# Optimization experiments

Hardware: AMD Instinct MI355X
Metric: run time of the kernel (lower is better)

Reference implementation:

```python
import jax, jax.numpy as jnp
import numpy as np

D_MODEL = 768
N_HEADS = 12
D_HEAD = D_MODEL // N_HEADS

def setup_inputs() -> dict:
    key = jax.random.key(0)
    ks = jax.random.split(key, 5)
    B, T = 2, 4096
    x = jax.random.normal(ks[0], (B, T, D_MODEL), dtype=jnp.float32)
    s_in = 1.0 / np.sqrt(D_MODEL)
    W_qkv = jax.random.normal(ks[1], (D_MODEL, 3 * D_MODEL), dtype=jnp.float32) * s_in
    b_qkv = jnp.zeros((3 * D_MODEL,), dtype=jnp.float32)
    W_proj = jax.random.normal(ks[2], (D_MODEL, D_MODEL), dtype=jnp.float32) * s_in
    b_proj = jnp.zeros((D_MODEL,), dtype=jnp.float32)
    return {"x": x, "W_qkv": W_qkv, "b_qkv": b_qkv, "W_proj": W_proj, "b_proj": b_proj}

def reference(x, W_qkv, b_qkv, W_proj, b_proj):
    B, T, C = x.shape
    qkv = x @ W_qkv + b_qkv                      # [B,T,3C]
    q, k, v = jnp.split(qkv, 3, axis=-1)
    def heads(t):
        return t.reshape(B, T, N_HEADS, D_HEAD).transpose(0, 2, 1, 3)  # [B,H,T,d]
    q, k, v = heads(q), heads(k), heads(v)
    scale = 1.0 / np.sqrt(D_HEAD)
    att = jnp.einsum('bhqd,bhkd->bhqk', q, k) * scale  # [B,H,T,T]
    causal = jnp.tril(jnp.ones((T, T), dtype=bool))
    att = jnp.where(causal[None, None], att, -jnp.inf)
    att = jax.nn.softmax(att, axis=-1)
    y = jnp.einsum('bhqk,bhkd->bhqd', att, v)          # [B,H,T,d]
    y = y.transpose(0, 2, 1, 3).reshape(B, T, C)
    return y @ W_proj + b_proj
```

## Files before the change

kernel.cpp:

```cpp
#include <hip/hip_runtime.h>
#include <hip/hip_bf16.h>

typedef __bf16 bf16_t;
typedef bf16_t bf16x4 __attribute__((ext_vector_type(4)));
typedef bf16_t bf16x8 __attribute__((ext_vector_type(8)));
typedef float  f32x4  __attribute__((ext_vector_type(4)));

#define TSEQ   4096
#define NBATCH 2
#define DMODEL 768
#define NHEADS 12
#define DHEAD  64
#define NTOK   (NBATCH*TSEQ)
#define NQKV   (3*DMODEL)

#define QSCALE 0.18033688011112042f
#define SMAX 24.0f

__device__ __forceinline__ f32x4 mfma16(bf16x8 a, bf16x8 b, f32x4 c) {
  return __builtin_amdgcn_mfma_f32_16x16x32_bf16(a, b, c, 0, 0, 0);
}

__device__ __forceinline__ void glds16(const bf16_t* g, bf16_t* l) {
  __builtin_amdgcn_global_load_lds(
      (const __attribute__((address_space(1))) void*)g,
      (__attribute__((address_space(3))) void*)l, 16, 0, 0);
}

__global__ __launch_bounds__(256) void k_prep(
    const float* __restrict__ W1, bf16_t* __restrict__ O1,
    const float* __restrict__ W2, bf16_t* __restrict__ O2,
    const float* __restrict__ X, bf16_t* __restrict__ Xb) {
  __shared__ bf16_t tile[64][66];
  int t = blockIdx.x;
  if (t >= 576) {
    const int idx = (t - 576) * 256 + threadIdx.x;
#pragma unroll
    for (int it = 0; it < 2; ++it) {
      const long c = (long)idx + (long)it * 393216;
      const float4 v0 = *(const float4*)(X + c * 8);
      const float4 v1 = *(const float4*)(X + c * 8 + 4);
      bf16x8 o;
      o[0] = (bf16_t)v0.x; o[1] = (bf16_t)v0.y;
      o[2] = (bf16_t)v0.z; o[3] = (bf16_t)v0.w;
      o[4] = (bf16_t)v1.x; o[5] = (bf16_t)v1.y;
      o[6] = (bf16_t)v1.z; o[7] = (bf16_t)v1.w;
      *(bf16x8*)(Xb + c * 8) = o;
    }
    return;
  }
  const float* in; bf16_t* out; int R, C, c0, r0;
  if (t < 432) { in = W1; out = O1; R = DMODEL; C = NQKV;
                 c0 = (t % 36) * 64; r0 = (t / 36) * 64; }
  else { t -= 432; in = W2; out = O2; R = DMODEL; C = DMODEL;
         c0 = (t % 12) * 64; r0 = (t / 12) * 64; }
  const int tid = threadIdx.x;
  const int r = tid >> 2, cb = (tid & 3) * 16;
  const float* ip = in + (long)(r0 + r) * C + c0 + cb;
#pragma unroll
  for (int k = 0; k < 16; k += 4) {
    float4 v = *(const float4*)(ip + k);
    tile[r][cb + k + 0] = (bf16_t)v.x;
    tile[r][cb + k + 1] = (bf16_t)v.y;
    tile[r][cb + k + 2] = (bf16_t)v.z;
    tile[r][cb + k + 3] = (bf16_t)v.w;
  }
  __syncthreads();
  const int c = tid >> 2, rb = (tid & 3) * 16;
  bf16_t* op = out + (long)(c0 + c) * R + r0 + rb;
  bf16x8 v0, v1;
#pragma unroll
  for (int i = 0; i < 8; ++i) { v0[i] = tile[rb + i][c]; v1[i] = tile[rb + 8 + i][c]; }
  *(bf16x8*)(op) = v0;
  *(bf16x8*)(op + 8) = v1;
}

__global__ __launch_bounds__(256) void k_gemm_qkv(
    const bf16_t* __restrict__ Xb, const bf16_t* __restrict__ Bt,
    const float* __restrict__ bias,
    bf16_t* __restrict__ Qo, bf16_t* __restrict__ Ko, bf16_t* __restrict__ Vt) {
  __shared__ __align__(16) bf16_t As[2 * 128 * 32];
  __shared__ __align__(16) bf16_t Bs[2 * 128 * 32];
  const int wave = threadIdx.x >> 6;
  const int lane = threadIdx.x & 63;
  const int quad = lane >> 4;
  const int l16  = lane & 15;
  const int m0 = blockIdx.x * 128;
  const int n0 = blockIdx.y * 128;

  const int srow4  = lane >> 2;
  const int schunk = (lane & 3) ^ ((lane >> 3) & 3);
  const bf16_t* a0 = Xb + (long)(m0 + wave * 32 + srow4) * DMODEL + schunk * 8;
  const bf16_t* b0 = Bt + (long)(n0 + wave * 32 + srow4) * DMODEL + schunk * 8;

  f32x4 acc[2][8] = {};

  glds16(a0,               As + (wave * 32) * 32);
  glds16(a0 + 16 * DMODEL, As + (wave * 32 + 16) * 32);
  glds16(b0,               Bs + (wave * 32) * 32);
  glds16(b0 + 16 * DMODEL, Bs + (wave * 32 + 16) * 32);
  __syncthreads();

  const int sw = (l16 >> 1) & 3;
  for (int ks = 0; ks < DMODEL / 32; ++ks) {
    const int p = ks & 1;
    if (ks + 1 < DMODEL / 32) {
      const int k1 = (ks + 1) * 32;
      bf16_t* Asx = (p ? As : As + 128 * 32);
      bf16_t* Bsx = (p ? Bs : Bs + 128 * 32);
      glds16(a0 + k1,               Asx + (wave * 32) * 32);
      glds16(a0 + 16 * DMODEL + k1, Asx + (wave * 32 + 16) * 32);
      glds16(b0 + k1,               Bsx + (wave * 32) * 32);
      glds16(b0 + 16 * DMODEL + k1, Bsx + (wave * 32 + 16) * 32);
    }
    const bf16_t* Ap = As + p * (128 * 32);
    const bf16_t* Bp = Bs + p * (128 * 32);

    bf16x8 af0 = *(const bf16x8*)(Ap + (wave * 32 + l16) * 32 + ((quad ^ sw) << 3));
    bf16x8 af1 = *(const bf16x8*)(Ap + (wave * 32 + 16 + l16) * 32 + ((quad ^ sw) << 3));
#pragma unroll
    for (int nt = 0; nt < 8; ++nt) {
      bf16x8 bfm = *(const bf16x8*)(Bp + (nt * 16 + l16) * 32 + ((quad ^ sw) << 3));
      acc[0][nt] = mfma16(af0, bfm, acc[0][nt]);
      acc[1][nt] = mfma16(af1, bfm, acc[1][nt]);
    }
    __syncthreads();
  }

#pragma unroll
  for (int s = 0; s < 2; ++s)
#pragma unroll
    for (int nt = 0; nt < 8; ++nt) {
      const int n = n0 + nt * 16 + l16;
      const float bv = bias[n];
      const int mb = m0 + wave * 32 + s * 16 + quad * 4;
      const int b = mb >> 12;
      const int t = mb & 4095;
      if (n < DMODEL) {
        const int h = n >> 6, d = n & 63;
        bf16_t* qp = Qo + (((long)(b * NHEADS + h) * TSEQ + t) << 6) + d;
#pragma unroll
        for (int j = 0; j < 4; ++j)
          qp[(long)j << 6] = (bf16_t)((acc[s][nt][j] + bv) * QSCALE);
      } else if (n < 2 * DMODEL) {
        const int n2 = n - DMODEL, h = n2 >> 6, d = n2 & 63;
        bf16_t* kp = Ko + (((long)(b * NHEADS + h) * TSEQ + t) << 6) + d;
#pragma unroll
        for (int j = 0; j < 4; ++j)
          kp[(long)j << 6] = (bf16_t)(acc[s][nt][j] + bv);
      } else {
        const int n2 = n - 2 * DMODEL, h = n2 >> 6, d = n2 & 63;
        bf16x4 v;
#pragma unroll
        for (int j = 0; j < 4; ++j) v[j] = (bf16_t)(acc[s][nt][j] + bv);
        *(bf16x4*)(Vt + ((long)(b * NHEADS + h) * DHEAD + d) * TSEQ + t) = v;
      }
    }
}

__global__ __launch_bounds__(256) void k_combine(
    const bf16_t* __restrict__ P0, const bf16_t* __restrict__ P1,
    const float* __restrict__ L0, const float* __restrict__ L1,
    bf16_t* __restrict__ Ab) {
  const int bh = blockIdx.x;
  const int t  = blockIdx.y * 32 + (threadIdx.x >> 3);
  const int d0 = (threadIdx.x & 7) * 8;
  const long lidx = (long)bh * TSEQ + t;
  const float li = 1.f / (L0[lidx] + L1[lidx]);
  const long pidx = (lidx << 6) + d0;
  bf16x8 a = *(const bf16x8*)(P0 + pidx);
  bf16x8 b = *(const bf16x8*)(P1 + pidx);
  bf16x8 o;
#pragma unroll
  for (int j = 0; j < 8; ++j)
    o[j] = (bf16_t)(((float)a[j] + (float)b[j]) * li);
  const int bb = bh / NHEADS, h = bh % NHEADS;
  *(bf16x8*)(Ab + (long)(bb * TSEQ + t) * DMODEL + h * 64 + d0) = o;
}

__global__ __launch_bounds__(256) void k_gemm_proj(
    const bf16_t* __restrict__ Ab, const bf16_t* __restrict__ Bt,
    const float* __restrict__ bias, float* __restrict__ out) {
  __shared__ __align__(16) bf16_t As[2 * 128 * 32];
  __shared__ __align__(16) bf16_t Bs[2 * 128 * 32];
  const int wave = threadIdx.x >> 6;
  const int lane = threadIdx.x & 63;
  const int quad = lane >> 4;
  const int l16  = lane & 15;
  const int m0 = blockIdx.x * 128;
  const int n0 = blockIdx.y * 128;

  const int srow4  = lane >> 2;
  const int schunk = (lane & 3) ^ ((lane >> 3) & 3);
  const bf16_t* a0 = Ab + (long)(m0 + wave * 32 + srow4) * DMODEL + schunk * 8;
  const bf16_t* b0 = Bt + (long)(n0 + wave * 32 + srow4) * DMODEL + schunk * 8;

  f32x4 acc[2][8] = {};

  glds16(a0,               As + (wave * 32) * 32);
  glds16(a0 + 16 * DMODEL, As + (wave * 32 + 16) * 32);
  glds16(b0,               Bs + (wave * 32) * 32);
  glds16(b0 + 16 * DMODEL, Bs + (wave * 32 + 16) * 32);
  __syncthreads();

  const int sw = (l16 >> 1) & 3;
  for (int ks = 0; ks < DMODEL / 32; ++ks) {
    const int p = ks & 1;
    if (ks + 1 < DMODEL / 32) {
      const int k1 = (ks + 1) * 32;
      bf16_t* Asx = (p ? As : As + 128 * 32);
      bf16_t* Bsx = (p ? Bs : Bs + 128 * 32);
      glds16(a0 + k1,               Asx + (wave * 32) * 32);
      glds16(a0 + 16 * DMODEL + k1, Asx + (wave * 32 + 16) * 32);
      glds16(b0 + k1,               Bsx + (wave * 32) * 32);
      glds16(b0 + 16 * DMODEL + k1, Bsx + (wave * 32 + 16) * 32);
    }
    const bf16_t* Ap = As + p * (128 * 32);
    const bf16_t* Bp = Bs + p * (128 * 32);

    bf16x8 af0 = *(const bf16x8*)(Ap + (wave * 32 + l16) * 32 + ((quad ^ sw) << 3));
    bf16x8 af1 = *(const bf16x8*)(Ap + (wave * 32 + 16 + l16) * 32 + ((quad ^ sw) << 3));
#pragma unroll
    for (int nt = 0; nt < 8; ++nt) {
      bf16x8 bfm = *(const bf16x8*)(Bp + (nt * 16 + l16) * 32 + ((quad ^ sw) << 3));
      acc[0][nt] = mfma16(af0, bfm, acc[0][nt]);
      acc[1][nt] = mfma16(af1, bfm, acc[1][nt]);
    }
    __syncthreads();
  }

#pragma unroll
  for (int s = 0; s < 2; ++s)
#pragma unroll
    for (int nt = 0; nt < 8; ++nt) {
      const int n = n0 + nt * 16 + l16;
      const float bv = bias[n];
      const int m = m0 + wave * 32 + s * 16 + quad * 4;
#pragma unroll
      for (int j = 0; j < 4; ++j)
        out[(long)(m + j) * DMODEL + n] = acc[s][nt][j] + bv;
    }
}

__global__ __launch_bounds__(256, 4) void k_attn(
    const bf16_t* __restrict__ Q, const bf16_t* __restrict__ K,
    const bf16_t* __restrict__ Vt,
    bf16_t* __restrict__ P0, bf16_t* __restrict__ P1,
    float* __restrict__ L0, float* __restrict__ L1) {
  __shared__ __align__(16) bf16_t kbuf[2][64 * 64];
  __shared__ __align__(16) bf16_t vbuf[2][64 * 64];
  const int wave = threadIdx.x >> 6;
  const int lane = threadIdx.x & 63;
  const int quad = lane >> 4;
  const int l16  = lane & 15;
  const int bh = blockIdx.x;
  const int qt = 31 - (blockIdx.y >> 1);
  const int sp = blockIdx.y & 1;
  const int niter = qt + 1;
  const int c0 = sp * niter;
  bf16_t* Pp = sp ? P1 : P0;
  float*  Lp = sp ? L1 : L0;

  const bf16_t* Qh = Q + ((long)bh * TSEQ << 6);
  const bf16_t* Kh = K + ((long)bh * TSEQ << 6);
  const bf16_t* Vh = Vt + (long)bh * DHEAD * TSEQ;

  const int qbase = qt * 128 + wave * 32;

  bf16x8 qf[2][2];
#pragma unroll
  for (int s = 0; s < 2; ++s) {
    const bf16_t* qrow = Qh + ((long)(qbase + s * 16 + l16) << 6);
    qf[s][0] = *(const bf16x8*)(qrow + quad * 8);
    qf[s][1] = *(const bf16x8*)(qrow + 32 + quad * 8);
  }

  f32x4 acc[2][4] = {};
  float lS[2] = {0.f, 0.f};
  const f32x4 minit = {-SMAX, -SMAX, -SMAX, -SMAX};

  const int kperm = ((l16 >> 2) << 3) + (l16 & 3);
  const int swl = l16 & 7;
  const int srow = lane >> 3;
  const int cV = (lane & 7) ^ (srow & 7);
  const int cK0 = (lane & 7) ^ (srow & 3);
  const int cK1 = cK0 ^ 4;
  const int r0a = wave * 16, r0b = wave * 16 + 8;

  {
    const int k00 = c0 << 6;
    glds16(Kh + ((long)(k00 + r0a + srow) << 6) + cK0 * 8, &kbuf[0][r0a * 64]);
    glds16(Kh + ((long)(k00 + r0b + srow) << 6) + cK1 * 8, &kbuf[0][r0b * 64]);
    glds16(Vh + (long)(r0a + srow) * TSEQ + k00 + cV * 8,  &vbuf[0][r0a * 64]);
    glds16(Vh + (long)(r0b + srow) * TSEQ + k00 + cV * 8,  &vbuf[0][r0b * 64]);
  }
  __syncthreads();

  for (int ci = 0; ci < niter; ++ci) {
    const int p = ci & 1;
    const int k0 = (c0 + ci) << 6;
    if (ci + 1 < niter) {
      const int k1 = k0 + 64;
      glds16(Kh + ((long)(k1 + r0a + srow) << 6) + cK0 * 8, &kbuf[1 - p][r0a * 64]);
      glds16(Kh + ((long)(k1 + r0b + srow) << 6) + cK1 * 8, &kbuf[1 - p][r0b * 64]);
      glds16(Vh + (long)(r0a + srow) * TSEQ + k1 + cV * 8,  &vbuf[1 - p][r0a * 64]);
      glds16(Vh + (long)(r0b + srow) * TSEQ + k1 + cV * 8,  &vbuf[1 - p][r0b * 64]);
    }
    const bf16_t* kb = kbuf[p];
    const bf16_t* vb = vbuf[p];

#pragma unroll
    for (int g = 0; g < 2; ++g) {
      const int rw0 = (g * 32 + kperm) * 64;
      const int rw1 = (g * 32 + 4 + kperm) * 64;
      bf16x8 kf00 = *(const bf16x8*)(kb + rw0 + ((quad ^ swl) << 3));
      bf16x8 kf01 = *(const bf16x8*)(kb + rw0 + (((quad + 4) ^ swl) << 3));
      bf16x8 kf10 = *(const bf16x8*)(kb + rw1 + ((quad ^ swl) << 3));
      bf16x8 kf11 = *(const bf16x8*)(kb + rw1 + (((quad + 4) ^ swl) << 3));
      const bool domask = (k0 + g * 32 + 31 > qbase);

      bf16x8 pf[2];
#pragma unroll
      for (int s = 0; s < 2; ++s) {
        f32x4 st0 = minit, st1 = minit;
        st0 = mfma16(kf00, qf[s][0], st0);
        st0 = mfma16(kf01, qf[s][1], st0);
        st1 = mfma16(kf10, qf[s][0], st1);
        st1 = mfma16(kf11, qf[s][1], st1);
        if (domask) {
          const int qS = qbase + s * 16 + l16;
          const int kb0 = k0 + g * 32 + quad * 8;
#pragma unroll
          for (int j = 0; j < 4; ++j) {
            if (kb0 + j > qS)     st0[j] = -1e30f;
            if (kb0 + 4 + j > qS) st1[j] = -1e30f;
          }
        }
        float rs = 0.f;
#pragma unroll
        for (int j = 0; j < 4; ++j) {
          float e0 = __builtin_amdgcn_exp2f(st0[j]);
          float e1 = __builtin_amdgcn_exp2f(st1[j]);
          rs += e0 + e1;
          pf[s][j]     = (bf16_t)e0;
          pf[s][4 + j] = (bf16_t)e1;
        }
        lS[s] += rs;
      }
#pragma unroll
      for (int dt = 0; dt < 4; ++dt) {
        const int row = dt * 16 + l16;
        bf16x8 vf = *(const bf16x8*)(vb + row * 64 + ((((g << 2) + quad) ^ swl) << 3));
#pragma unroll
        for (int s = 0; s < 2; ++s)
          acc[s][dt] = mfma16(vf, pf[s], acc[s][dt]);
      }
    }
    __syncthreads();
  }

#pragma unroll
  for (int s = 0; s < 2; ++s) {
    lS[s] += __shfl_xor(lS[s], 16);
    lS[s] += __shfl_xor(lS[s], 32);
  }
#pragma unroll
  for (int s = 0; s < 2; ++s) {
    const int qS = qbase + s * 16 + l16;
    bf16_t* prow = Pp + (((long)bh * TSEQ + qS) << 6);
#pragma unroll
    for (int dt = 0; dt < 4; ++dt) {
      bf16x4 w;
#pragma unroll
      for (int j = 0; j < 4; ++j) w[j] = (bf16_t)acc[s][dt][j];
      *(bf16x4*)(prow + dt * 16 + quad * 4) = w;
    }
    if (quad == 0) Lp[(long)bh * TSEQ + qS] = lS[s];
  }
}

extern "C" void kernel_launch(void* const* d_in, const int* in_sizes, int n_in,
                              void* d_out, int out_size, void* d_ws, size_t ws_size,
                              hipStream_t stream) {
  (void)in_sizes; (void)n_in; (void)out_size; (void)ws_size;
  const float* x     = (const float*)d_in[0];
  const float* Wqkv  = (const float*)d_in[1];
  const float* bqkv  = (const float*)d_in[2];
  const float* Wproj = (const float*)d_in[3];
  const float* bproj = (const float*)d_in[4];
  float* out = (float*)d_out;

  char* ws = (char*)d_ws;
  bf16_t* wqkv_t  = (bf16_t*)ws; ws += (long)NQKV * DMODEL * 2;
  bf16_t* wproj_t = (bf16_t*)ws; ws += (long)DMODEL * DMODEL * 2;
  bf16_t* Xb      = (bf16_t*)ws; ws += (long)NTOK * DMODEL * 2;
  bf16_t* Qb      = (bf16_t*)ws; ws += (long)NTOK * DMODEL * 2;
  bf16_t* Kb      = (bf16_t*)ws; ws += (long)NTOK * DMODEL * 2;
  bf16_t* Vtb     = (bf16_t*)ws; ws += (long)NTOK * DMODEL * 2;
  bf16_t* P0b     = (bf16_t*)ws; ws += (long)NTOK * DMODEL * 2;
  bf16_t* P1b     = (bf16_t*)ws; ws += (long)NTOK * DMODEL * 2;
  bf16_t* Abb     = (bf16_t*)ws; ws += (long)NTOK * DMODEL * 2;
  float*  L0b     = (float*)ws;  ws += (long)NHEADS * NBATCH * TSEQ * 4;
  float*  L1b     = (float*)ws;  ws += (long)NHEADS * NBATCH * TSEQ * 4;

  k_prep<<<576 + 1536, 256, 0, stream>>>(Wqkv, wqkv_t, Wproj, wproj_t, x, Xb);
  k_gemm_qkv<<<dim3(NTOK / 128, NQKV / 128), 256, 0, stream>>>(Xb, wqkv_t, bqkv, Qb, Kb, Vtb);
  k_attn<<<dim3(NBATCH * NHEADS, 64), 256, 0, stream>>>(Qb, Kb, Vtb, P0b, P1b, L0b, L1b);
  k_combine<<<dim3(NBATCH * NHEADS, TSEQ / 32), 256, 0, stream>>>(
      P0b, P1b, L0b, L1b, Abb);
  k_gemm_proj<<<dim3(NTOK / 128, DMODEL / 128), 256, 0, stream>>>(
      Abb, wproj_t, bproj, out);
}
```

Measured before the change: 221.9 us.

## Drop split-KV attention with combine kernel; triple-buffer QKV GEMM loads

The attention kernel no longer splits each query tile's causal KV range across two blocks. Each block now processes the whole range and normalizes its output directly into the projection input, which removes the combine kernel and the partial-output and log-sum buffers. Separately, the QKV GEMM moves from double to triple-buffered LDS staging with explicit vmcnt waits and raw barriers, so loads for the next two k-slices stay in flight. The cost is half as many attention blocks (768 versus 1536) with long, unbalanced per-block work, so tail imbalance and lower occupancy may hurt.

```diff
diff --git a/kernel.cpp b/kernel.cpp
--- a/kernel.cpp
+++ b/kernel.cpp
@@ -79,6 +79,99 @@
     const bf16_t* __restrict__ Xb, const bf16_t* __restrict__ Bt,
     const float* __restrict__ bias,
     bf16_t* __restrict__ Qo, bf16_t* __restrict__ Ko, bf16_t* __restrict__ Vt) {
+  __shared__ __align__(16) bf16_t As[3 * 128 * 32];
+  __shared__ __align__(16) bf16_t Bs[3 * 128 * 32];
+  const int wave = threadIdx.x >> 6;
+  const int lane = threadIdx.x & 63;
+  const int quad = lane >> 4;
+  const int l16  = lane & 15;
+  const int m0 = blockIdx.x * 128;
+  const int n0 = blockIdx.y * 128;
+
+  const int srow4  = lane >> 2;
+  const int schunk = (lane & 3) ^ ((lane >> 3) & 3);
+  const bf16_t* a0 = Xb + (long)(m0 + wave * 32 + srow4) * DMODEL + schunk * 8;
+  const bf16_t* b0 = Bt + (long)(n0 + wave * 32 + srow4) * DMODEL + schunk * 8;
+
+  f32x4 acc[2][8] = {};
+
+  auto stage = [&](int ks) {
+    const int koff = ks * 32;
+    bf16_t* Ax = As + (ks % 3) * (128 * 32);
+    bf16_t* Bx = Bs + (ks % 3) * (128 * 32);
+    glds16(a0 + koff,               Ax + (wave * 32) * 32);
+    glds16(a0 + 16 * DMODEL + koff, Ax + (wave * 32 + 16) * 32);
+    glds16(b0 + koff,               Bx + (wave * 32) * 32);
+    glds16(b0 + 16 * DMODEL + koff, Bx + (wave * 32 + 16) * 32);
+  };
+
+  const int NS = DMODEL / 32;
+  stage(0);
+  stage(1);
+  asm volatile("s_waitcnt vmcnt(4)" ::: "memory");
+  __builtin_amdgcn_s_barrier();
+  __builtin_amdgcn_sched_barrier(0);
+
+  const int sw = (l16 >> 1) & 3;
+  for (int ks = 0; ks < NS; ++ks) {
+    if (ks + 2 < NS) stage(ks + 2);
+    const bf16_t* Ap = As + (ks % 3) * (128 * 32);
+    const bf16_t* Bp = Bs + (ks % 3) * (128 * 32);
+
+    bf16x8 af0 = *(const bf16x8*)(Ap + (wave * 32 + l16) * 32 + ((quad ^ sw) << 3));
+    bf16x8 af1 = *(const bf16x8*)(Ap + (wave * 32 + 16 + l16) * 32 + ((quad ^ sw) << 3));
+#pragma unroll
+    for (int nt = 0; nt < 8; ++nt) {
+      bf16x8 bfm = *(const bf16x8*)(Bp + (nt * 16 + l16) * 32 + ((quad ^ sw) << 3));
+      acc[0][nt] = mfma16(af0, bfm, acc[0][nt]);
+      acc[1][nt] = mfma16(af1, bfm, acc[1][nt]);
+    }
+
+    if (ks + 1 < NS) {
+      if (ks + 2 < NS) {
+        asm volatile("s_waitcnt vmcnt(4)" ::: "memory");
+      } else {
+        asm volatile("s_waitcnt vmcnt(0)" ::: "memory");
+      }
+      __builtin_amdgcn_s_barrier();
+      __builtin_amdgcn_sched_barrier(0);
+    }
+  }
+
+#pragma unroll
+  for (int s = 0; s < 2; ++s)
+#pragma unroll
+    for (int nt = 0; nt < 8; ++nt) {
+      const int n = n0 + nt * 16 + l16;
+      const float bv = bias[n];
+      const int mb = m0 + wave * 32 + s * 16 + quad * 4;
+      const int b = mb >> 12;
+      const int t = mb & 4095;
+      if (n < DMODEL) {
+        const int h = n >> 6, d = n & 63;
+        bf16_t* qp = Qo + (((long)(b * NHEADS + h) * TSEQ + t) << 6) + d;
+#pragma unroll
+        for (int j = 0; j < 4; ++j)
+          qp[(long)j << 6] = (bf16_t)((acc[s][nt][j] + bv) * QSCALE);
+      } else if (n < 2 * DMODEL) {
+        const int n2 = n - DMODEL, h = n2 >> 6, d = n2 & 63;
+        bf16_t* kp = Ko + (((long)(b * NHEADS + h) * TSEQ + t) << 6) + d;
+#pragma unroll
+        for (int j = 0; j < 4; ++j)
+          kp[(long)j << 6] = (bf16_t)(acc[s][nt][j] + bv);
+      } else {
+        const int n2 = n - 2 * DMODEL, h = n2 >> 6, d = n2 & 63;
+        bf16x4 v;
+#pragma unroll
+        for (int j = 0; j < 4; ++j) v[j] = (bf16_t)(acc[s][nt][j] + bv);
+        *(bf16x4*)(Vt + ((long)(b * NHEADS + h) * DHEAD + d) * TSEQ + t) = v;
+      }
+    }
+}
+
+__global__ __launch_bounds__(256) void k_gemm_proj(
+    const bf16_t* __restrict__ Ab, const bf16_t* __restrict__ Bt,
+    const float* __restrict__ bias, float* __restrict__ out) {
   __shared__ __align__(16) bf16_t As[2 * 128 * 32];
   __shared__ __align__(16) bf16_t Bs[2 * 128 * 32];
   const int wave = threadIdx.x >> 6;
@@ -90,7 +183,7 @@
 
   const int srow4  = lane >> 2;
   const int schunk = (lane & 3) ^ ((lane >> 3) & 3);
-  const bf16_t* a0 = Xb + (long)(m0 + wave * 32 + srow4) * DMODEL + schunk * 8;
+  const bf16_t* a0 = Ab + (long)(m0 + wave * 32 + srow4) * DMODEL + schunk * 8;
   const bf16_t* b0 = Bt + (long)(n0 + wave * 32 + srow4) * DMODEL + schunk * 8;
 
   f32x4 acc[2][8] = {};
@@ -133,108 +226,6 @@
     for (int nt = 0; nt < 8; ++nt) {
       const int n = n0 + nt * 16 + l16;
       const float bv = bias[n];
-      const int mb = m0 + wave * 32 + s * 16 + quad * 4;
-      const int b = mb >> 12;
-      const int t = mb & 4095;
-      if (n < DMODEL) {
-        const int h = n >> 6, d = n & 63;
-        bf16_t* qp = Qo + (((long)(b * NHEADS + h) * TSEQ + t) << 6) + d;
-#pragma unroll
-        for (int j = 0; j < 4; ++j)
-          qp[(long)j << 6] = (bf16_t)((acc[s][nt][j] + bv) * QSCALE);
-      } else if (n < 2 * DMODEL) {
-        const int n2 = n - DMODEL, h = n2 >> 6, d = n2 & 63;
-        bf16_t* kp = Ko + (((long)(b * NHEADS + h) * TSEQ + t) << 6) + d;
-#pragma unroll
-        for (int j = 0; j < 4; ++j)
-          kp[(long)j << 6] = (bf16_t)(acc[s][nt][j] + bv);
-      } else {
-        const int n2 = n - 2 * DMODEL, h = n2 >> 6, d = n2 & 63;
-        bf16x4 v;
-#pragma unroll
-        for (int j = 0; j < 4; ++j) v[j] = (bf16_t)(acc[s][nt][j] + bv);
-        *(bf16x4*)(Vt + ((long)(b * NHEADS + h) * DHEAD + d) * TSEQ + t) = v;
-      }
-    }
-}
-
-__global__ __launch_bounds__(256) void k_combine(
-    const bf16_t* __restrict__ P0, const bf16_t* __restrict__ P1,
-    const float* __restrict__ L0, const float* __restrict__ L1,
-    bf16_t* __restrict__ Ab) {
-  const int bh = blockIdx.x;
-  const int t  = blockIdx.y * 32 + (threadIdx.x >> 3);
-  const int d0 = (threadIdx.x & 7) * 8;
-  const long lidx = (long)bh * TSEQ + t;
-  const float li = 1.f / (L0[lidx] + L1[lidx]);
-  const long pidx = (lidx << 6) + d0;
-  bf16x8 a = *(const bf16x8*)(P0 + pidx);
-  bf16x8 b = *(const bf16x8*)(P1 + pidx);
-  bf16x8 o;
-#pragma unroll
-  for (int j = 0; j < 8; ++j)
-    o[j] = (bf16_t)(((float)a[j] + (float)b[j]) * li);
-  const int bb = bh / NHEADS, h = bh % NHEADS;
-  *(bf16x8*)(Ab + (long)(bb * TSEQ + t) * DMODEL + h * 64 + d0) = o;
-}
-
-__global__ __launch_bounds__(256) void k_gemm_proj(
-    const bf16_t* __restrict__ Ab, const bf16_t* __restrict__ Bt,
-    const float* __restrict__ bias, float* __restrict__ out) {
-  __shared__ __align__(16) bf16_t As[2 * 128 * 32];
-  __shared__ __align__(16) bf16_t Bs[2 * 128 * 32];
-  const int wave = threadIdx.x >> 6;
-  const int lane = threadIdx.x & 63;
-  const int quad = lane >> 4;
-  const int l16  = lane & 15;
-  const int m0 = blockIdx.x * 128;
-  const int n0 = blockIdx.y * 128;
-
-  const int srow4  = lane >> 2;
-  const int schunk = (lane & 3) ^ ((lane >> 3) & 3);
-  const bf16_t* a0 = Ab + (long)(m0 + wave * 32 + srow4) * DMODEL + schunk * 8;
-  const bf16_t* b0 = Bt + (long)(n0 + wave * 32 + srow4) * DMODEL + schunk * 8;
-
-  f32x4 acc[2][8] = {};
-
-  glds16(a0,               As + (wave * 32) * 32);
-  glds16(a0 + 16 * DMODEL, As + (wave * 32 + 16) * 32);
-  glds16(b0,               Bs + (wave * 32) * 32);
-  glds16(b0 + 16 * DMODEL, Bs + (wave * 32 + 16) * 32);
-  __syncthreads();
-
-  const int sw = (l16 >> 1) & 3;
-  for (int ks = 0; ks < DMODEL / 32; ++ks) {
-    const int p = ks & 1;
-    if (ks + 1 < DMODEL / 32) {
-      const int k1 = (ks + 1) * 32;
-      bf16_t* Asx = (p ? As : As + 128 * 32);
-      bf16_t* Bsx = (p ? Bs : Bs + 128 * 32);
-      glds16(a0 + k1,               Asx + (wave * 32) * 32);
-      glds16(a0 + 16 * DMODEL + k1, Asx + (wave * 32 + 16) * 32);
-      glds16(b0 + k1,               Bsx + (wave * 32) * 32);
-      glds16(b0 + 16 * DMODEL + k1, Bsx + (wave * 32 + 16) * 32);
-    }
-    const bf16_t* Ap = As + p * (128 * 32);
-    const bf16_t* Bp = Bs + p * (128 * 32);
-
-    bf16x8 af0 = *(const bf16x8*)(Ap + (wave * 32 + l16) * 32 + ((quad ^ sw) << 3));
-    bf16x8 af1 = *(const bf16x8*)(Ap + (wave * 32 + 16 + l16) * 32 + ((quad ^ sw) << 3));
-#pragma unroll
-    for (int nt = 0; nt < 8; ++nt) {
-      bf16x8 bfm = *(const bf16x8*)(Bp + (nt * 16 + l16) * 32 + ((quad ^ sw) << 3));
-      acc[0][nt] = mfma16(af0, bfm, acc[0][nt]);
-      acc[1][nt] = mfma16(af1, bfm, acc[1][nt]);
-    }
-    __syncthreads();
-  }
-
-#pragma unroll
-  for (int s = 0; s < 2; ++s)
-#pragma unroll
-    for (int nt = 0; nt < 8; ++nt) {
-      const int n = n0 + nt * 16 + l16;
-      const float bv = bias[n];
       const int m = m0 + wave * 32 + s * 16 + quad * 4;
 #pragma unroll
       for (int j = 0; j < 4; ++j)
@@ -244,9 +235,7 @@
 
 __global__ __launch_bounds__(256, 4) void k_attn(
     const bf16_t* __restrict__ Q, const bf16_t* __restrict__ K,
-    const bf16_t* __restrict__ Vt,
-    bf16_t* __restrict__ P0, bf16_t* __restrict__ P1,
-    float* __restrict__ L0, float* __restrict__ L1) {
+    const bf16_t* __restrict__ Vt, bf16_t* __restrict__ Ab) {
   __shared__ __align__(16) bf16_t kbuf[2][64 * 64];
   __shared__ __align__(16) bf16_t vbuf[2][64 * 64];
   const int wave = threadIdx.x >> 6;
@@ -254,12 +243,8 @@
   const int quad = lane >> 4;
   const int l16  = lane & 15;
   const int bh = blockIdx.x;
-  const int qt = 31 - (blockIdx.y >> 1);
-  const int sp = blockIdx.y & 1;
-  const int niter = qt + 1;
-  const int c0 = sp * niter;
-  bf16_t* Pp = sp ? P1 : P0;
-  float*  Lp = sp ? L1 : L0;
+  const int qt = 31 - blockIdx.y;
+  const int niter = 2 * qt + 2;
 
   const bf16_t* Qh = Q + ((long)bh * TSEQ << 6);
   const bf16_t* Kh = K + ((long)bh * TSEQ << 6);
@@ -288,17 +273,16 @@
   const int r0a = wave * 16, r0b = wave * 16 + 8;
 
   {
-    const int k00 = c0 << 6;
-    glds16(Kh + ((long)(k00 + r0a + srow) << 6) + cK0 * 8, &kbuf[0][r0a * 64]);
-    glds16(Kh + ((long)(k00 + r0b + srow) << 6) + cK1 * 8, &kbuf[0][r0b * 64]);
-    glds16(Vh + (long)(r0a + srow) * TSEQ + k00 + cV * 8,  &vbuf[0][r0a * 64]);
-    glds16(Vh + (long)(r0b + srow) * TSEQ + k00 + cV * 8,  &vbuf[0][r0b * 64]);
+    glds16(Kh + ((long)(r0a + srow) << 6) + cK0 * 8, &kbuf[0][r0a * 64]);
+    glds16(Kh + ((long)(r0b + srow) << 6) + cK1 * 8, &kbuf[0][r0b * 64]);
+    glds16(Vh + (long)(r0a + srow) * TSEQ + cV * 8,  &vbuf[0][r0a * 64]);
+    glds16(Vh + (long)(r0b + srow) * TSEQ + cV * 8,  &vbuf[0][r0b * 64]);
   }
   __syncthreads();
 
   for (int ci = 0; ci < niter; ++ci) {
     const int p = ci & 1;
-    const int k0 = (c0 + ci) << 6;
+    const int k0 = ci << 6;
     if (ci + 1 < niter) {
       const int k1 = k0 + 64;
       glds16(Kh + ((long)(k1 + r0a + srow) << 6) + cK0 * 8, &kbuf[1 - p][r0a * 64]);
@@ -364,18 +348,19 @@
     lS[s] += __shfl_xor(lS[s], 16);
     lS[s] += __shfl_xor(lS[s], 32);
   }
+  const int bb = bh / NHEADS, h = bh % NHEADS;
 #pragma unroll
   for (int s = 0; s < 2; ++s) {
     const int qS = qbase + s * 16 + l16;
-    bf16_t* prow = Pp + (((long)bh * TSEQ + qS) << 6);
+    const float linv = 1.f / lS[s];
+    bf16_t* arow = Ab + (long)(bb * TSEQ + qS) * DMODEL + h * 64;
 #pragma unroll
     for (int dt = 0; dt < 4; ++dt) {
       bf16x4 w;
 #pragma unroll
-      for (int j = 0; j < 4; ++j) w[j] = (bf16_t)acc[s][dt][j];
-      *(bf16x4*)(prow + dt * 16 + quad * 4) = w;
-    }
-    if (quad == 0) Lp[(long)bh * TSEQ + qS] = lS[s];
+      for (int j = 0; j < 4; ++j) w[j] = (bf16_t)(acc[s][dt][j] * linv);
+      *(bf16x4*)(arow + dt * 16 + quad * 4) = w;
+    }
   }
 }
 
@@ -397,17 +382,11 @@
   bf16_t* Qb      = (bf16_t*)ws; ws += (long)NTOK * DMODEL * 2;
   bf16_t* Kb      = (bf16_t*)ws; ws += (long)NTOK * DMODEL * 2;
   bf16_t* Vtb     = (bf16_t*)ws; ws += (long)NTOK * DMODEL * 2;
-  bf16_t* P0b     = (bf16_t*)ws; ws += (long)NTOK * DMODEL * 2;
-  bf16_t* P1b     = (bf16_t*)ws; ws += (long)NTOK * DMODEL * 2;
   bf16_t* Abb     = (bf16_t*)ws; ws += (long)NTOK * DMODEL * 2;
-  float*  L0b     = (float*)ws;  ws += (long)NHEADS * NBATCH * TSEQ * 4;
-  float*  L1b     = (float*)ws;  ws += (long)NHEADS * NBATCH * TSEQ * 4;
 
   k_prep<<<576 + 1536, 256, 0, stream>>>(Wqkv, wqkv_t, Wproj, wproj_t, x, Xb);
   k_gemm_qkv<<<dim3(NTOK / 128, NQKV / 128), 256, 0, stream>>>(Xb, wqkv_t, bqkv, Qb, Kb, Vtb);
-  k_attn<<<dim3(NBATCH * NHEADS, 64), 256, 0, stream>>>(Qb, Kb, Vtb, P0b, P1b, L0b, L1b);
-  k_combine<<<dim3(NBATCH * NHEADS, TSEQ / 32), 256, 0, stream>>>(
-      P0b, P1b, L0b, L1b, Abb);
+  k_attn<<<dim3(NBATCH * NHEADS, 32), 256, 0, stream>>>(Qb, Kb, Vtb, Abb);
   k_gemm_proj<<<dim3(NTOK / 128, DMODEL / 128), 256, 0, stream>>>(
       Abb, wproj_t, bproj, out);
 }
```

Result: slower. 226.5 us (+2.1%).

## Triple-buffer QKV GEMM loads and shrink proj GEMM tile to 64x128

Applied to the files above, without the earlier changes.

The QKV GEMM moves from a double-buffered LDS pipeline with a full __syncthreads per k-step to a three-stage ring. It prefetches two stages ahead and uses partial vmcnt waits plus raw s_barrier, so global-to-LDS loads overlap more compute. The projection GEMM is retiled from 128x128 to 64x128 with each wave owning 32 output columns, which doubles the block count to fill more CUs. It also sets launch bounds to allow 6 blocks per CU. The cost is more LDS in the QKV kernel and less per-block reuse in the projection.

```diff
diff --git a/kernel.cpp b/kernel.cpp
--- a/kernel.cpp
+++ b/kernel.cpp
@@ -79,8 +79,8 @@
     const bf16_t* __restrict__ Xb, const bf16_t* __restrict__ Bt,
     const float* __restrict__ bias,
     bf16_t* __restrict__ Qo, bf16_t* __restrict__ Ko, bf16_t* __restrict__ Vt) {
-  __shared__ __align__(16) bf16_t As[2 * 128 * 32];
-  __shared__ __align__(16) bf16_t Bs[2 * 128 * 32];
+  __shared__ __align__(16) bf16_t As[3 * 128 * 32];
+  __shared__ __align__(16) bf16_t Bs[3 * 128 * 32];
   const int wave = threadIdx.x >> 6;
   const int lane = threadIdx.x & 63;
   const int quad = lane >> 4;
@@ -95,26 +95,28 @@
 
   f32x4 acc[2][8] = {};
 
-  glds16(a0,               As + (wave * 32) * 32);
-  glds16(a0 + 16 * DMODEL, As + (wave * 32 + 16) * 32);
-  glds16(b0,               Bs + (wave * 32) * 32);
-  glds16(b0 + 16 * DMODEL, Bs + (wave * 32 + 16) * 32);
-  __syncthreads();
+  auto stage = [&](int ks) {
+    const int koff = ks * 32;
+    bf16_t* Ax = As + (ks % 3) * (128 * 32);
+    bf16_t* Bx = Bs + (ks % 3) * (128 * 32);
+    glds16(a0 + koff,               Ax + (wave * 32) * 32);
+    glds16(a0 + 16 * DMODEL + koff, Ax + (wave * 32 + 16) * 32);
+    glds16(b0 + koff,               Bx + (wave * 32) * 32);
+    glds16(b0 + 16 * DMODEL + koff, Bx + (wave * 32 + 16) * 32);
+  };
+
+  const int NS = DMODEL / 32;
+  stage(0);
+  stage(1);
+  asm volatile("s_waitcnt vmcnt(4)" ::: "memory");
+  __builtin_amdgcn_s_barrier();
+  __builtin_amdgcn_sched_barrier(0);
 
   const int sw = (l16 >> 1) & 3;
-  for (int ks = 0; ks < DMODEL / 32; ++ks) {
-    const int p = ks & 1;
-    if (ks + 1 < DMODEL / 32) {
-      const int k1 = (ks + 1) * 32;
-      bf16_t* Asx = (p ? As : As + 128 * 32);
-      bf16_t* Bsx = (p ? Bs : Bs + 128 * 32);
-      glds16(a0 + k1,               Asx + (wave * 32) * 32);
-      glds16(a0 + 16 * DMODEL + k1, Asx + (wave * 32 + 16) * 32);
-      glds16(b0 + k1,               Bsx + (wave * 32) * 32);
-      glds16(b0 + 16 * DMODEL + k1, Bsx + (wave * 32 + 16) * 32);
-    }
-    const bf16_t* Ap = As + p * (128 * 32);
-    const bf16_t* Bp = Bs + p * (128 * 32);
+  for (int ks = 0; ks < NS; ++ks) {
+    if (ks + 2 < NS) stage(ks + 2);
+    const bf16_t* Ap = As + (ks % 3) * (128 * 32);
+    const bf16_t* Bp = Bs + (ks % 3) * (128 * 32);
 
     bf16x8 af0 = *(const bf16x8*)(Ap + (wave * 32 + l16) * 32 + ((quad ^ sw) << 3));
     bf16x8 af1 = *(const bf16x8*)(Ap + (wave * 32 + 16 + l16) * 32 + ((quad ^ sw) << 3));
@@ -124,7 +126,16 @@
       acc[0][nt] = mfma16(af0, bfm, acc[0][nt]);
       acc[1][nt] = mfma16(af1, bfm, acc[1][nt]);
     }
-    __syncthreads();
+
+    if (ks + 1 < NS) {
+      if (ks + 2 < NS) {
+        asm volatile("s_waitcnt vmcnt(4)" ::: "memory");
+      } else {
+        asm volatile("s_waitcnt vmcnt(0)" ::: "memory");
+      }
+      __builtin_amdgcn_s_barrier();
+      __builtin_amdgcn_sched_barrier(0);
+    }
   }
 
 #pragma unroll
@@ -178,27 +189,26 @@
   *(bf16x8*)(Ab + (long)(bb * TSEQ + t) * DMODEL + h * 64 + d0) = o;
 }
 
-__global__ __launch_bounds__(256) void k_gemm_proj(
+__global__ __launch_bounds__(256, 6) void k_gemm_proj(
     const bf16_t* __restrict__ Ab, const bf16_t* __restrict__ Bt,
     const float* __restrict__ bias, float* __restrict__ out) {
-  __shared__ __align__(16) bf16_t As[2 * 128 * 32];
+  __shared__ __align__(16) bf16_t As[2 * 64 * 32];
   __shared__ __align__(16) bf16_t Bs[2 * 128 * 32];
   const int wave = threadIdx.x >> 6;
   const int lane = threadIdx.x & 63;
   const int quad = lane >> 4;
   const int l16  = lane & 15;
-  const int m0 = blockIdx.x * 128;
+  const int m0 = blockIdx.x * 64;
   const int n0 = blockIdx.y * 128;
 
   const int srow4  = lane >> 2;
   const int schunk = (lane & 3) ^ ((lane >> 3) & 3);
-  const bf16_t* a0 = Ab + (long)(m0 + wave * 32 + srow4) * DMODEL + schunk * 8;
+  const bf16_t* a0 = Ab + (long)(m0 + wave * 16 + srow4) * DMODEL + schunk * 8;
   const bf16_t* b0 = Bt + (long)(n0 + wave * 32 + srow4) * DMODEL + schunk * 8;
 
-  f32x4 acc[2][8] = {};
-
-  glds16(a0,               As + (wave * 32) * 32);
-  glds16(a0 + 16 * DMODEL, As + (wave * 32 + 16) * 32);
+  f32x4 acc[2][4] = {};
+
+  glds16(a0,               As + (wave * 16) * 32);
   glds16(b0,               Bs + (wave * 32) * 32);
   glds16(b0 + 16 * DMODEL, Bs + (wave * 32 + 16) * 32);
   __syncthreads();
@@ -208,37 +218,36 @@
     const int p = ks & 1;
     if (ks + 1 < DMODEL / 32) {
       const int k1 = (ks + 1) * 32;
-      bf16_t* Asx = (p ? As : As + 128 * 32);
-      bf16_t* Bsx = (p ? Bs : Bs + 128 * 32);
-      glds16(a0 + k1,               Asx + (wave * 32) * 32);
-      glds16(a0 + 16 * DMODEL + k1, Asx + (wave * 32 + 16) * 32);
-      glds16(b0 + k1,               Bsx + (wave * 32) * 32);
-      glds16(b0 + 16 * DMODEL + k1, Bsx + (wave * 32 + 16) * 32);
-    }
-    const bf16_t* Ap = As + p * (128 * 32);
+      bf16_t* Ax = (p ? As : As + 64 * 32);
+      bf16_t* Bx = (p ? Bs : Bs + 128 * 32);
+      glds16(a0 + k1,               Ax + (wave * 16) * 32);
+      glds16(b0 + k1,               Bx + (wave * 32) * 32);
+      glds16(b0 + 16 * DMODEL + k1, Bx + (wave * 32 + 16) * 32);
+    }
+    const bf16_t* Ap = As + p * (64 * 32);
     const bf16_t* Bp = Bs + p * (128 * 32);
 
-    bf16x8 af0 = *(const bf16x8*)(Ap + (wave * 32 + l16) * 32 + ((quad ^ sw) << 3));
-    bf16x8 af1 = *(const bf16x8*)(Ap + (wave * 32 + 16 + l16) * 32 + ((quad ^ sw) << 3));
-#pragma unroll
-    for (int nt = 0; nt < 8; ++nt) {
-      bf16x8 bfm = *(const bf16x8*)(Bp + (nt * 16 + l16) * 32 + ((quad ^ sw) << 3));
-      acc[0][nt] = mfma16(af0, bfm, acc[0][nt]);
-      acc[1][nt] = mfma16(af1, bfm, acc[1][nt]);
+    bf16x8 bf0 = *(const bf16x8*)(Bp + (wave * 32 + l16) * 32 + ((quad ^ sw) << 3));
+    bf16x8 bf1 = *(const bf16x8*)(Bp + (wave * 32 + 16 + l16) * 32 + ((quad ^ sw) << 3));
+#pragma unroll
+    for (int mf = 0; mf < 4; ++mf) {
+      bf16x8 af = *(const bf16x8*)(Ap + (mf * 16 + l16) * 32 + ((quad ^ sw) << 3));
+      acc[0][mf] = mfma16(af, bf0, acc[0][mf]);
+      acc[1][mf] = mfma16(af, bf1, acc[1][mf]);
     }
     __syncthreads();
   }
 
 #pragma unroll
-  for (int s = 0; s < 2; ++s)
-#pragma unroll
-    for (int nt = 0; nt < 8; ++nt) {
-      const int n = n0 + nt * 16 + l16;
+  for (int nf = 0; nf < 2; ++nf)
+#pragma unroll
+    for (int mf = 0; mf < 4; ++mf) {
+      const int n = n0 + wave * 32 + nf * 16 + l16;
       const float bv = bias[n];
-      const int m = m0 + wave * 32 + s * 16 + quad * 4;
+      const int m = m0 + mf * 16 + quad * 4;
 #pragma unroll
       for (int j = 0; j < 4; ++j)
-        out[(long)(m + j) * DMODEL + n] = acc[s][nt][j] + bv;
+        out[(long)(m + j) * DMODEL + n] = acc[nf][mf][j] + bv;
     }
 }
 
@@ -408,6 +417,6 @@
   k_attn<<<dim3(NBATCH * NHEADS, 64), 256, 0, stream>>>(Qb, Kb, Vtb, P0b, P1b, L0b, L1b);
   k_combine<<<dim3(NBATCH * NHEADS, TSEQ / 32), 256, 0, stream>>>(
       P0b, P1b, L0b, L1b, Abb);
-  k_gemm_proj<<<dim3(NTOK / 128, DMODEL / 128), 256, 0, stream>>>(
+  k_gemm_proj<<<dim3(NTOK / 64, DMODEL / 128), 256, 0, stream>>>(
       Abb, wproj_t, bproj, out);
 }
```

Result: no change. 220.9 us (-0.5%).
